# Kernel optimization log

Hardware: AMD Instinct MI355X
Metric: run time of the kernel (lower is better)

Reference implementation:

```python
import jax, jax.numpy as jnp
import numpy as np
import math

B, T, C, H = 4, 2048, 1024, 16
HS = C // H
EPS = 1e-5


def layernorm(x, g, b):
    mu = jnp.mean(x, axis=-1, keepdims=True)
    var = jnp.var(x, axis=-1, keepdims=True)
    return (x - mu) * jax.lax.rsqrt(var + EPS) * g + b


def setup_inputs() -> dict:
    key = jax.random.key(0)
    ks = jax.random.split(key, 7)
    rn = lambda k, s: jax.random.normal(k, s, dtype=jnp.float32) * 0.02
    return {
        "x": jax.random.normal(ks[0], (B, T, C), dtype=jnp.float32),
        "mask": jnp.tril(jnp.ones((T, T), dtype=jnp.int32)),  # causal tril buffer
        "wq": rn(ks[1], (H, HS, C)),  # stacked per-head Linear weights [out,in]
        "wk": rn(ks[2], (H, HS, C)),
        "wv": rn(ks[3], (H, HS, C)),
        "ln1_g": jnp.ones((C,), jnp.float32),
        "ln1_b": jnp.zeros((C,), jnp.float32),
        "ln2_g": jnp.ones((C,), jnp.float32),
        "ln2_b": jnp.zeros((C,), jnp.float32),
        "w1": rn(ks[4], (4 * C, C)),
        "b1": jnp.zeros((4 * C,), jnp.float32),
        "w2": rn(ks[5], (C, 4 * C)),
        "b2": jnp.zeros((C,), jnp.float32),
    }


def reference(x, mask, wq, wk, wv, ln1_g, ln1_b, ln2_g, ln2_b, w1, b1, w2, b2):
    Bx, Tx, Cx = x.shape
    h = layernorm(x, ln1_g, ln1_b)
    # per-head projections, batched over heads: [B,H,T,HS]
    q = jnp.einsum('btc,hdc->bhtd', h, wq)
    k = jnp.einsum('btc,hdc->bhtd', h, wk)
    v = jnp.einsum('btc,hdc->bhtd', h, wv)
    scores = jnp.einsum('bhtd,bhsd->bhts', q, k) * (1.0 / math.sqrt(HS))
    scores = jnp.where(mask[None, None, :Tx, :Tx] == 0, -jnp.inf, scores)
    w = jax.nn.softmax(scores, axis=-1)
    attn = jnp.einsum('bhts,bhsd->bhtd', w, v)  # [B,H,T,HS]
    attn = attn.transpose(0, 2, 1, 3).reshape(Bx, Tx, Cx)  # concat heads
    x = x + attn
    h2 = layernorm(x, ln2_g, ln2_b)
    ff = jax.nn.silu(h2 @ w1.T + b1) @ w2.T + b2  # dropout = identity (eval)
    return x + ff
```

## Files before the change

kernel.cpp:

```cpp
#include <hip/hip_runtime.h>
#include <stdint.h>

#define Bb 4
#define Tt 2048
#define Cc 1024
#define Hh 16
#define HSs 64

typedef __attribute__((ext_vector_type(8))) __bf16 bf16x8;
typedef __attribute__((ext_vector_type(4))) float f32x4;

__device__ __forceinline__ ushort f2bf(float f){
  union { float f; uint u; } c; c.f = f;
  uint r = c.u + 0x7fffu + ((c.u >> 16) & 1u);
  return (ushort)(r >> 16);
}
__device__ __forceinline__ float bf2f(ushort u){
  union { uint u; float f; } c; c.u = ((uint)u) << 16; return c.f;
}

__device__ __forceinline__ void gload16(const void* g, void* l){
  __builtin_amdgcn_global_load_lds(
      (__attribute__((address_space(1))) void*)(g),
      (__attribute__((address_space(3))) void*)(l), 16, 0, 0);
}

__global__ __launch_bounds__(256) void cast_bf16_kernel(const float* __restrict__ in,
                                                        ushort* __restrict__ out){
  int i = (blockIdx.x * 256 + threadIdx.x) * 4;
  float4 v = *(const float4*)(in + i);
  ushort4 o; o.x = f2bf(v.x); o.y = f2bf(v.y); o.z = f2bf(v.z); o.w = f2bf(v.w);
  *(ushort4*)(out + i) = o;
}

__global__ __launch_bounds__(256) void ln1_kernel(const float* __restrict__ x,
    const float* __restrict__ gw, const float* __restrict__ bw,
    ushort* __restrict__ hout){
  int row = blockIdx.x, tid = threadIdx.x;
  size_t base = (size_t)row * Cc + tid * 4;
  float4 xv = *(const float4*)(x + base);
  float s  = xv.x + xv.y + xv.z + xv.w;
  float ss = xv.x*xv.x + xv.y*xv.y + xv.z*xv.z + xv.w*xv.w;
  #pragma unroll
  for (int off = 1; off < 64; off <<= 1){ s += __shfl_xor(s, off); ss += __shfl_xor(ss, off); }
  __shared__ float red[8];
  int wid = tid >> 6, lane = tid & 63;
  if (lane == 0){ red[wid] = s; red[4 + wid] = ss; }
  __syncthreads();
  s  = red[0] + red[1] + red[2] + red[3];
  ss = red[4] + red[5] + red[6] + red[7];
  float mu = s * (1.0f / Cc);
  float rstd = rsqrtf(ss * (1.0f / Cc) - mu * mu + 1e-5f);
  float4 gv = *(const float4*)(gw + tid * 4);
  float4 bv = *(const float4*)(bw + tid * 4);
  ushort4 o;
  o.x = f2bf((xv.x - mu) * rstd * gv.x + bv.x);
  o.y = f2bf((xv.y - mu) * rstd * gv.y + bv.y);
  o.z = f2bf((xv.z - mu) * rstd * gv.z + bv.z);
  o.w = f2bf((xv.w - mu) * rstd * gv.w + bv.w);
  *(ushort4*)(hout + base) = o;
}

__global__ __launch_bounds__(256) void ln2_kernel(const float* __restrict__ x,
    const ushort* __restrict__ attnb,
    const float* __restrict__ gw, const float* __restrict__ bw,
    float* __restrict__ x2, ushort* __restrict__ hout){
  int row = blockIdx.x, tid = threadIdx.x;
  size_t base = (size_t)row * Cc + tid * 4;
  float4 xv = *(const float4*)(x + base);
  ushort4 av = *(const ushort4*)(attnb + base);
  xv.x += bf2f(av.x); xv.y += bf2f(av.y); xv.z += bf2f(av.z); xv.w += bf2f(av.w);
  *(float4*)(x2 + base) = xv;
  float s  = xv.x + xv.y + xv.z + xv.w;
  float ss = xv.x*xv.x + xv.y*xv.y + xv.z*xv.z + xv.w*xv.w;
  #pragma unroll
  for (int off = 1; off < 64; off <<= 1){ s += __shfl_xor(s, off); ss += __shfl_xor(ss, off); }
  __shared__ float red[8];
  int wid = tid >> 6, lane = tid & 63;
  if (lane == 0){ red[wid] = s; red[4 + wid] = ss; }
  __syncthreads();
  s  = red[0] + red[1] + red[2] + red[3];
  ss = red[4] + red[5] + red[6] + red[7];
  float mu = s * (1.0f / Cc);
  float rstd = rsqrtf(ss * (1.0f / Cc) - mu * mu + 1e-5f);
  float4 gv = *(const float4*)(gw + tid * 4);
  float4 bv = *(const float4*)(bw + tid * 4);
  ushort4 o;
  o.x = f2bf((xv.x - mu) * rstd * gv.x + bv.x);
  o.y = f2bf((xv.y - mu) * rstd * gv.y + bv.y);
  o.z = f2bf((xv.z - mu) * rstd * gv.z + bv.z);
  o.w = f2bf((xv.w - mu) * rstd * gv.w + bv.w);
  *(ushort4*)(hout + base) = o;
}

#define MFMA_QUAD(SI, QI, BQ) \
  { \
    _Pragma("unroll") \
    for (int mi = 0; mi < 4; ++mi){ \
      acc[(SI)*4+mi][(QI)*2+0] = __builtin_amdgcn_mfma_f32_16x16x32_bf16(af[mi][0], BQ[0][0], acc[(SI)*4+mi][(QI)*2+0], 0,0,0); \
      acc[(SI)*4+mi][(QI)*2+0] = __builtin_amdgcn_mfma_f32_16x16x32_bf16(af[mi][1], BQ[0][1], acc[(SI)*4+mi][(QI)*2+0], 0,0,0); \
      acc[(SI)*4+mi][(QI)*2+1] = __builtin_amdgcn_mfma_f32_16x16x32_bf16(af[mi][0], BQ[1][0], acc[(SI)*4+mi][(QI)*2+1], 0,0,0); \
      acc[(SI)*4+mi][(QI)*2+1] = __builtin_amdgcn_mfma_f32_16x16x32_bf16(af[mi][1], BQ[1][1], acc[(SI)*4+mi][(QI)*2+1], 0,0,0); \
    } \
  }

#define PH_SYNC_PRE()  { __builtin_amdgcn_sched_barrier(0); __builtin_amdgcn_s_barrier(); \
                         asm volatile("s_waitcnt lgkmcnt(0)" ::: "memory"); \
                         __builtin_amdgcn_sched_barrier(0); __builtin_amdgcn_s_setprio(1); }
#define PH_SYNC_POST() { __builtin_amdgcn_s_setprio(0); __builtin_amdgcn_sched_barrier(0); \
                         __builtin_amdgcn_s_barrier(); }

template<int MODE>
__global__ __launch_bounds__(512, 2) void gemm256_kernel(
    const ushort* __restrict__ A, const ushort* __restrict__ Bw,
    int N, int K,
    ushort* __restrict__ obf, float* __restrict__ of32,
    const float* __restrict__ bias)
{
  __shared__ __align__(16) ushort lds[2][2][2][128 * 64];
  int tid = threadIdx.x, lane = tid & 63, wid = tid >> 6;
  int wm = wid >> 2, wn = wid & 3;
  int c = lane & 15, g = lane >> 4;

  int nwg = gridDim.x, bid = blockIdx.x;
  int wgid = (bid & 7) * (nwg >> 3) + (bid >> 3);
  int m0, n0, koff = 0;
  if (MODE == 3){
    int split = wgid >> 7, rem = wgid & 127;
    m0 = (rem >> 2) << 8; n0 = (rem & 3) << 8; koff = split << 11;
  } else {
    int nTn = N >> 8;
    m0 = (wgid / nTn) << 8; n0 = (wgid % nTn) << 8;
  }

  const ushort* Ag = A  + (size_t)m0 * K + koff;
  const ushort* Bg = Bw + (size_t)n0 * K + koff;

  auto stage = [&](const ushort* gbase, int t, int ab, int h){
    #pragma unroll
    for (int j = 0; j < 2; ++j){
      int d = j * 8192 + wid * 1024 + lane * 16;
      int row = d >> 7;
      int colb = (d & 127) ^ ((row & 7) << 4);
      gload16((const char*)gbase + ((size_t)(h * 128 + row) * K + t * 64) * 2 + colb,
              (char*)&lds[t & 1][ab][h][0] + j * 8192 + wid * 1024);
    }
  };

  f32x4 acc[8][4] = {};
  bf16x8 af[4][2], bq0[2][2], bq1[2][2];
  int nt = (MODE == 3) ? (K >> 7) : (K >> 6);

  stage(Ag, 0, 0, 0); stage(Ag, 0, 0, 1);
  stage(Bg, 0, 1, 0); stage(Bg, 0, 1, 1);
  stage(Bg, 1, 1, 0); stage(Bg, 1, 1, 1);
  asm volatile("s_waitcnt vmcnt(4)" ::: "memory");
  __builtin_amdgcn_sched_barrier(0);
  __builtin_amdgcn_s_barrier();

  for (int t = 0; t < nt; ++t){
    const char* Abuf = (const char*)&lds[t & 1][0][wm][0];
    const char* Bbuf = (const char*)&lds[t & 1][1][wn >> 1][0];
    int brow0 = (wn & 1) * 64;

    #pragma unroll
    for (int mi = 0; mi < 4; ++mi){
      int row = mi * 16 + c, sw = (row & 7) << 4;
      af[mi][0] = *(const bf16x8*)(Abuf + row * 128 + ((g * 16) ^ sw));
      af[mi][1] = *(const bf16x8*)(Abuf + row * 128 + ((64 + g * 16) ^ sw));
    }
    #pragma unroll
    for (int nj = 0; nj < 2; ++nj){
      int row = brow0 + nj * 16 + c, sw = (row & 7) << 4;
      bq0[nj][0] = *(const bf16x8*)(Bbuf + row * 128 + ((g * 16) ^ sw));
      bq0[nj][1] = *(const bf16x8*)(Bbuf + row * 128 + ((64 + g * 16) ^ sw));
    }
    if (t + 1 < nt) stage(Ag, t + 1, 0, 0);
    PH_SYNC_PRE();
    MFMA_QUAD(0, 0, bq0);
    PH_SYNC_POST();

    #pragma unroll
    for (int nj = 0; nj < 2; ++nj){
      int row = brow0 + 32 + nj * 16 + c, sw = (row & 7) << 4;
      bq1[nj][0] = *(const bf16x8*)(Bbuf + row * 128 + ((g * 16) ^ sw));
      bq1[nj][1] = *(const bf16x8*)(Bbuf + row * 128 + ((64 + g * 16) ^ sw));
    }
    if (t + 1 < nt) stage(Ag, t + 1, 0, 1);
    PH_SYNC_PRE();
    MFMA_QUAD(0, 1, bq1);
    PH_SYNC_POST();

    #pragma unroll
    for (int mi = 0; mi < 4; ++mi){
      int row = 64 + mi * 16 + c, sw = (row & 7) << 4;
      af[mi][0] = *(const bf16x8*)(Abuf + row * 128 + ((g * 16) ^ sw));
      af[mi][1] = *(const bf16x8*)(Abuf + row * 128 + ((64 + g * 16) ^ sw));
    }
    if (t + 2 < nt) stage(Bg, t + 2, 1, 0);
    PH_SYNC_PRE();
    MFMA_QUAD(1, 0, bq0);
    PH_SYNC_POST();

    if (t + 2 < nt){
      stage(Bg, t + 2, 1, 1);
      asm volatile("s_waitcnt vmcnt(4)" ::: "memory");
    } else {
      asm volatile("s_waitcnt vmcnt(0)" ::: "memory");
    }
    __builtin_amdgcn_sched_barrier(0);
    __builtin_amdgcn_s_barrier();
    __builtin_amdgcn_s_setprio(1);
    MFMA_QUAD(1, 1, bq1);
    PH_SYNC_POST();
  }

  #pragma unroll
  for (int mi = 0; mi < 8; ++mi){
    #pragma unroll
    for (int ni = 0; ni < 4; ++ni){
      #pragma unroll
      for (int r = 0; r < 4; ++r){
        float v = acc[mi][ni][r];
        int m = m0 + wm * 128 + mi * 16 + g * 4 + r;
        int n = n0 + wn * 64 + ni * 16 + c;
        if (MODE == 0){
          int which = n >> 10;
          int nn = n & 1023;
          int b = m >> 11, t = m & (Tt - 1);
          int h = nn >> 6, d = nn & 63;
          float vv = (which == 0) ? v * 0.125f : v;
          size_t base = (size_t)which * (size_t)(Bb * Tt * Cc);
          size_t idx = (which == 2)
              ? ((((size_t)(b * Hh + h)) * HSs + d) * Tt + t)
              : ((((size_t)(b * Hh + h)) * Tt + t) * HSs + d);
          obf[base + idx] = f2bf(vv);
        } else if (MODE == 1){
          v += bias[n];
          float sv = v / (1.0f + __expf(-v));
          obf[(size_t)m * N + n] = f2bf(sv);
        } else {
          if (koff == 0) v += bias[n];
          atomicAdd(&of32[(size_t)m * N + n], v);
        }
      }
    }
  }
}

__global__ __launch_bounds__(256, 2) void attn_kernel(
    const ushort* __restrict__ q, const ushort* __restrict__ k,
    const ushort* __restrict__ vt, ushort* __restrict__ attnb)
{
  __shared__ __align__(16) ushort Ksm[3][64 * 64];
  __shared__ __align__(16) ushort Vsm[3][64 * 64];
  __shared__ __align__(16) ushort Pl[4][32 * 64];

  int bh  = blockIdx.y;
  int p   = blockIdx.x;
  int tid = threadIdx.x, wid = tid >> 6, lane = tid & 63;
  int g = lane >> 4, c = lane & 15;
  int qbA = 15 - p, qbB = p;
  int q0A = qbA * 128 + wid * 32;
  int q0B = qbB * 128 + wid * 32;
  const ushort* Qb = q  + (size_t)bh * Tt * HSs;
  const ushort* Kb = k  + (size_t)bh * Tt * HSs;
  const ushort* Vt = vt + (size_t)bh * HSs * Tt;
  char* Pw = (char*)&Pl[wid][0];

  auto stageKV = [&](int bsel, int s0){
    #pragma unroll
    for (int half = 0; half < 2; ++half){
      int i = wid + half * 4;
      int row = i * 8 + (lane >> 3);
      int col = ((lane & 7) ^ (row & 7)) * 8;
      gload16(Kb + (size_t)(s0 + row) * HSs + col, &Ksm[bsel][i * 512]);
      gload16(Vt + (size_t)row * Tt + s0 + col,    &Vsm[bsel][i * 512]);
    }
  };

  bf16x8 qfA[2][2], qfB[2][2];
  #pragma unroll
  for (int mi = 0; mi < 2; ++mi)
    #pragma unroll
    for (int ks = 0; ks < 2; ++ks){
      qfA[mi][ks] = *(const bf16x8*)(Qb + (size_t)(q0A + mi * 16 + c) * HSs + ks * 32 + g * 8);
      qfB[mi][ks] = *(const bf16x8*)(Qb + (size_t)(q0B + mi * 16 + c) * HSs + ks * 32 + g * 8);
    }

  f32x4 oA[2][4] = {}, oB[2][4] = {};
  float mA[2][4], lA[2][4], mB[2][4], lB[2][4];
  #pragma unroll
  for (int mi = 0; mi < 2; ++mi)
    #pragma unroll
    for (int r = 0; r < 4; ++r){
      mA[mi][r] = -1e30f; lA[mi][r] = 0.f;
      mB[mi][r] = -1e30f; lB[mi][r] = 0.f;
    }

  auto computeTile = [&](bf16x8 (&qf)[2][2], f32x4 (&o)[2][4],
                         float (&mrow)[2][4], float (&lpart)[2][4],
                         int q0w, int s0, const char* Kbuf, const char* Vbuf){
    f32x4 S[2][4] = {};
    bf16x8 kf[4][2];
    #pragma unroll
    for (int ni = 0; ni < 4; ++ni)
      #pragma unroll
      for (int ks = 0; ks < 2; ++ks)
        kf[ni][ks] = *(const bf16x8*)(Kbuf + (ni * 16 + c) * 128 + (((ks * 4 + g) ^ (c & 7)) << 4));
    #pragma unroll
    for (int mi = 0; mi < 2; ++mi)
      #pragma unroll
      for (int ni = 0; ni < 4; ++ni)
        #pragma unroll
        for (int ks = 0; ks < 2; ++ks)
          S[mi][ni] = __builtin_amdgcn_mfma_f32_16x16x32_bf16(qf[mi][ks], kf[ni][ks], S[mi][ni], 0, 0, 0);

    if (s0 + 63 > q0w){
      #pragma unroll
      for (int mi = 0; mi < 2; ++mi)
        #pragma unroll
        for (int ni = 0; ni < 4; ++ni)
          #pragma unroll
          for (int r = 0; r < 4; ++r){
            int tl = q0w + mi * 16 + g * 4 + r, sl = s0 + ni * 16 + c;
            if (sl > tl) S[mi][ni][r] = -1e30f;
          }
    }

    float lmax[2][4], worst = -1e30f;
    #pragma unroll
    for (int mi = 0; mi < 2; ++mi)
      #pragma unroll
      for (int r = 0; r < 4; ++r){
        float a0 = fmaxf(S[mi][0][r], S[mi][1][r]);
        float a1 = fmaxf(S[mi][2][r], S[mi][3][r]);
        lmax[mi][r] = fmaxf(a0, a1);
        worst = fmaxf(worst, lmax[mi][r] - mrow[mi][r]);
      }
    if (!__all(worst <= 8.0f)){
      #pragma unroll
      for (int mi = 0; mi < 2; ++mi)
        #pragma unroll
        for (int r = 0; r < 4; ++r){
          float mx = lmax[mi][r];
          mx = fmaxf(mx, __shfl_xor(mx, 1));
          mx = fmaxf(mx, __shfl_xor(mx, 2));
          mx = fmaxf(mx, __shfl_xor(mx, 4));
          mx = fmaxf(mx, __shfl_xor(mx, 8));
          float mnew  = fmaxf(mrow[mi][r], mx);
          float alpha = __expf(mrow[mi][r] - mnew);
          lpart[mi][r] *= alpha;
          #pragma unroll
          for (int dt = 0; dt < 4; ++dt) o[mi][dt][r] *= alpha;
          mrow[mi][r] = mnew;
        }
    }
    #pragma unroll
    for (int mi = 0; mi < 2; ++mi)
      #pragma unroll
      for (int r = 0; r < 4; ++r){
        int row = mi * 16 + g * 4 + r;
        float mb = mrow[mi][r] * 1.44269504f;
        float pp[4];
        #pragma unroll
        for (int ni = 0; ni < 4; ++ni){
          pp[ni] = exp2f(__builtin_fmaf(S[mi][ni][r], 1.44269504f, -mb));
          *(ushort*)(Pw + row * 128 + (((ni * 32 + 2 * c) ^ ((row & 7) << 4)))) = f2bf(pp[ni]);
        }
        lpart[mi][r] += (pp[0] + pp[1]) + (pp[2] + pp[3]);
      }
    __builtin_amdgcn_sched_barrier(0);

    bf16x8 vf[4][2];
    #pragma unroll
    for (int dt = 0; dt < 4; ++dt)
      #pragma unroll
      for (int ks = 0; ks < 2; ++ks)
        vf[dt][ks] = *(const bf16x8*)(Vbuf + (dt * 16 + c) * 128 + (((ks * 4 + g) ^ (c & 7)) << 4));
    #pragma unroll
    for (int mi = 0; mi < 2; ++mi){
      #pragma unroll
      for (int ks = 0; ks < 2; ++ks){
        bf16x8 pf = *(const bf16x8*)(Pw + (mi * 16 + c) * 128 + ((((ks * 4 + g) ^ (c & 7)) << 4)));
        #pragma unroll
        for (int dt = 0; dt < 4; ++dt)
          o[mi][dt] = __builtin_amdgcn_mfma_f32_16x16x32_bf16(pf, vf[dt][ks], o[mi][dt], 0, 0, 0);
      }
    }
    __builtin_amdgcn_sched_barrier(0);
  };

  int nchA = 2 * qbA + 2;

  stageKV(0, 0);
  stageKV(1, 64);
  asm volatile("s_waitcnt vmcnt(4)" ::: "memory");
  __builtin_amdgcn_sched_barrier(0);
  __builtin_amdgcn_s_barrier();

  int bufC = 0;
  for (int ch = 0; ch < nchA; ++ch){
    int s0 = ch * 64;
    bool staged = (ch + 2 < nchA);
    if (staged) stageKV((bufC == 0) ? 2 : bufC - 1, s0 + 128);

    const char* Kbuf = (const char*)&Ksm[bufC][0];
    const char* Vbuf = (const char*)&Vsm[bufC][0];
    if (s0 <= q0A + 31)
      computeTile(qfA, oA, mA, lA, q0A, s0, Kbuf, Vbuf);
    if (s0 <= q0B + 31)
      computeTile(qfB, oB, mB, lB, q0B, s0, Kbuf, Vbuf);

    if (staged) asm volatile("s_waitcnt vmcnt(4)" ::: "memory");
    else        asm volatile("s_waitcnt vmcnt(0)" ::: "memory");
    __builtin_amdgcn_sched_barrier(0);
    __builtin_amdgcn_s_barrier();
    bufC = (bufC == 2) ? 0 : bufC + 1;
  }

  int b = bh >> 4, h = bh & 15;
  #pragma unroll
  for (int mi = 0; mi < 2; ++mi)
    #pragma unroll
    for (int r = 0; r < 4; ++r){
      float la = lA[mi][r];
      la += __shfl_xor(la, 1); la += __shfl_xor(la, 2);
      la += __shfl_xor(la, 4); la += __shfl_xor(la, 8);
      float lia = 1.0f / la;
      float lb = lB[mi][r];
      lb += __shfl_xor(lb, 1); lb += __shfl_xor(lb, 2);
      lb += __shfl_xor(lb, 4); lb += __shfl_xor(lb, 8);
      float lib = 1.0f / lb;
      #pragma unroll
      for (int dt = 0; dt < 4; ++dt){
        int tA = q0A + mi * 16 + g * 4 + r;
        int tB = q0B + mi * 16 + g * 4 + r;
        attnb[((size_t)(b * Tt + tA)) * Cc + h * HSs + dt * 16 + c] = f2bf(oA[mi][dt][r] * lia);
        attnb[((size_t)(b * Tt + tB)) * Cc + h * HSs + dt * 16 + c] = f2bf(oB[mi][dt][r] * lib);
      }
    }
}

extern "C" void kernel_launch(void* const* d_in, const int* in_sizes, int n_in,
                              void* d_out, int out_size, void* d_ws, size_t ws_size,
                              hipStream_t stream) {
  (void)in_sizes; (void)n_in; (void)out_size; (void)ws_size;
  const float* x    = (const float*)d_in[0];
  const float* wq   = (const float*)d_in[2];
  const float* wk   = (const float*)d_in[3];
  const float* wv   = (const float*)d_in[4];
  const float* ln1g = (const float*)d_in[5];
  const float* ln1b = (const float*)d_in[6];
  const float* ln2g = (const float*)d_in[7];
  const float* ln2b = (const float*)d_in[8];
  const float* w1   = (const float*)d_in[9];
  const float* b1   = (const float*)d_in[10];
  const float* w2   = (const float*)d_in[11];
  const float* b2   = (const float*)d_in[12];
  float* out = (float*)d_out;

  char* ws = (char*)d_ws;
  const size_t SZ_ACT = (size_t)Bb * Tt * Cc * 2;
  ushort* h1    = (ushort*)(ws);
  ushort* qbuf  = (ushort*)(ws + SZ_ACT);
  ushort* kbuf  = (ushort*)(ws + 2 * SZ_ACT);
  ushort* vbuf  = (ushort*)(ws + 3 * SZ_ACT);
  ushort* attnb = (ushort*)(ws + 4 * SZ_ACT);
  ushort* h2    = (ushort*)(ws + 5 * SZ_ACT);
  ushort* h3    = (ushort*)(ws + 6 * SZ_ACT);
  char*   wsw   = ws + 6 * SZ_ACT + (size_t)Bb * Tt * 4 * Cc * 2;
  ushort* wqb = (ushort*)(wsw);
  ushort* wkb = (ushort*)(wsw + (size_t)Cc * Cc * 2);
  ushort* wvb = (ushort*)(wsw + 2 * (size_t)Cc * Cc * 2);
  ushort* w1b = (ushort*)(wsw + 3 * (size_t)Cc * Cc * 2);
  ushort* w2b = (ushort*)(wsw + 3 * (size_t)Cc * Cc * 2 + (size_t)4 * Cc * Cc * 2);

  cast_bf16_kernel<<<dim3(Cc * Cc / 1024), 256, 0, stream>>>(wq, wqb);
  cast_bf16_kernel<<<dim3(Cc * Cc / 1024), 256, 0, stream>>>(wk, wkb);
  cast_bf16_kernel<<<dim3(Cc * Cc / 1024), 256, 0, stream>>>(wv, wvb);
  cast_bf16_kernel<<<dim3(4 * Cc * Cc / 1024), 256, 0, stream>>>(w1, w1b);
  cast_bf16_kernel<<<dim3(4 * Cc * Cc / 1024), 256, 0, stream>>>(w2, w2b);

  ln1_kernel<<<dim3(Bb * Tt), 256, 0, stream>>>(x, ln1g, ln1b, h1);

  gemm256_kernel<0><<<dim3(32 * 12), 512, 0, stream>>>(h1, wqb, 3 * Cc, Cc, qbuf, nullptr, nullptr);

  attn_kernel<<<dim3(8, Bb * Hh), 256, 0, stream>>>(qbuf, kbuf, vbuf, attnb);

  ln2_kernel<<<dim3(Bb * Tt), 256, 0, stream>>>(x, attnb, ln2g, ln2b, out, h2);

  gemm256_kernel<1><<<dim3(32 * 16), 512, 0, stream>>>(h2, w1b, 4 * Cc, Cc, h3, nullptr, b1);
  gemm256_kernel<3><<<dim3(256), 512, 0, stream>>>(h3, w2b, Cc, 4 * Cc, nullptr, out, b2);
}
```

Baseline: 426.5 us.

## Merge weight casts into one kernel, split FFN1 GEMM, drop attention sched barriers

```diff
diff --git a/kernel.cpp b/kernel.cpp
--- a/kernel.cpp
+++ b/kernel.cpp
@@ -25,10 +25,18 @@
       (__attribute__((address_space(3))) void*)(l), 16, 0, 0);
 }
 
-__global__ __launch_bounds__(256) void cast_bf16_kernel(const float* __restrict__ in,
-                                                        ushort* __restrict__ out){
+__global__ __launch_bounds__(256) void cast_all_kernel(
+    const float* __restrict__ wq, const float* __restrict__ wk,
+    const float* __restrict__ wv, const float* __restrict__ w1,
+    const float* __restrict__ w2, ushort* __restrict__ out){
   int i = (blockIdx.x * 256 + threadIdx.x) * 4;
-  float4 v = *(const float4*)(in + i);
+  const float* src; int off;
+  if      (i <  1048576){ src = wq; off = i; }
+  else if (i <  2097152){ src = wk; off = i - 1048576; }
+  else if (i <  3145728){ src = wv; off = i - 2097152; }
+  else if (i <  7340032){ src = w1; off = i - 3145728; }
+  else                  { src = w2; off = i - 7340032; }
+  float4 v = *(const float4*)(src + off);
   ushort4 o; o.x = f2bf(v.x); o.y = f2bf(v.y); o.z = f2bf(v.z); o.w = f2bf(v.w);
   *(ushort4*)(out + i) = o;
 }
@@ -111,9 +119,9 @@
                          __builtin_amdgcn_s_barrier(); }
 
 template<int MODE>
-__global__ __launch_bounds__(512, 2) void gemm256_kernel(
+__device__ __forceinline__ void gemm256_body(
     const ushort* __restrict__ A, const ushort* __restrict__ Bw,
-    int N, int K,
+    int N, int K, int ldO,
     ushort* __restrict__ obf, float* __restrict__ of32,
     const float* __restrict__ bias)
 {
@@ -238,7 +246,7 @@
         } else if (MODE == 1){
           v += bias[n];
           float sv = v / (1.0f + __expf(-v));
-          obf[(size_t)m * N + n] = f2bf(sv);
+          obf[(size_t)m * ldO + n] = f2bf(sv);
         } else {
           if (koff == 0) v += bias[n];
           atomicAdd(&of32[(size_t)m * N + n], v);
@@ -246,6 +254,22 @@
       }
     }
   }
+}
+
+__global__ __launch_bounds__(512, 2) void gemm_qkv_kernel(
+    const ushort* __restrict__ A, const ushort* __restrict__ Bw, int N, int K,
+    ushort* __restrict__ obf){
+  gemm256_body<0>(A, Bw, N, K, 0, obf, nullptr, nullptr);
+}
+__global__ __launch_bounds__(512, 2) void gemm_ffn1_kernel(
+    const ushort* __restrict__ A, const ushort* __restrict__ Bw, int N, int K, int ldO,
+    ushort* __restrict__ obf, const float* __restrict__ bias){
+  gemm256_body<1>(A, Bw, N, K, ldO, obf, nullptr, bias);
+}
+__global__ __launch_bounds__(512, 2) void gemm_ffn2_kernel(
+    const ushort* __restrict__ A, const ushort* __restrict__ Bw, int N, int K,
+    float* __restrict__ of32, const float* __restrict__ bias){
+  gemm256_body<3>(A, Bw, N, K, N, nullptr, of32, bias);
 }
 
 __global__ __launch_bounds__(256, 2) void attn_kernel(
@@ -370,7 +394,6 @@
         }
         lpart[mi][r] += (pp[0] + pp[1]) + (pp[2] + pp[3]);
       }
-    __builtin_amdgcn_sched_barrier(0);
 
     bf16x8 vf[4][2];
     #pragma unroll
@@ -388,7 +411,6 @@
           o[mi][dt] = __builtin_amdgcn_mfma_f32_16x16x32_bf16(pf, vf[dt][ks], o[mi][dt], 0, 0, 0);
       }
     }
-    __builtin_amdgcn_sched_barrier(0);
   };
 
   int nchA = 2 * qbA + 2;
@@ -471,25 +493,20 @@
   ushort* h3    = (ushort*)(ws + 6 * SZ_ACT);
   char*   wsw   = ws + 6 * SZ_ACT + (size_t)Bb * Tt * 4 * Cc * 2;
   ushort* wqb = (ushort*)(wsw);
-  ushort* wkb = (ushort*)(wsw + (size_t)Cc * Cc * 2);
-  ushort* wvb = (ushort*)(wsw + 2 * (size_t)Cc * Cc * 2);
   ushort* w1b = (ushort*)(wsw + 3 * (size_t)Cc * Cc * 2);
   ushort* w2b = (ushort*)(wsw + 3 * (size_t)Cc * Cc * 2 + (size_t)4 * Cc * Cc * 2);
 
-  cast_bf16_kernel<<<dim3(Cc * Cc / 1024), 256, 0, stream>>>(wq, wqb);
-  cast_bf16_kernel<<<dim3(Cc * Cc / 1024), 256, 0, stream>>>(wk, wkb);
-  cast_bf16_kernel<<<dim3(Cc * Cc / 1024), 256, 0, stream>>>(wv, wvb);
-  cast_bf16_kernel<<<dim3(4 * Cc * Cc / 1024), 256, 0, stream>>>(w1, w1b);
-  cast_bf16_kernel<<<dim3(4 * Cc * Cc / 1024), 256, 0, stream>>>(w2, w2b);
+  cast_all_kernel<<<dim3(11264), 256, 0, stream>>>(wq, wk, wv, w1, w2, wqb);
 
   ln1_kernel<<<dim3(Bb * Tt), 256, 0, stream>>>(x, ln1g, ln1b, h1);
 
-  gemm256_kernel<0><<<dim3(32 * 12), 512, 0, stream>>>(h1, wqb, 3 * Cc, Cc, qbuf, nullptr, nullptr);
+  gemm_qkv_kernel<<<dim3(32 * 12), 512, 0, stream>>>(h1, wqb, 3 * Cc, Cc, qbuf);
 
   attn_kernel<<<dim3(8, Bb * Hh), 256, 0, stream>>>(qbuf, kbuf, vbuf, attnb);
 
   ln2_kernel<<<dim3(Bb * Tt), 256, 0, stream>>>(x, attnb, ln2g, ln2b, out, h2);
 
-  gemm256_kernel<1><<<dim3(32 * 16), 512, 0, stream>>>(h2, w1b, 4 * Cc, Cc, h3, nullptr, b1);
-  gemm256_kernel<3><<<dim3(256), 512, 0, stream>>>(h3, w2b, Cc, 4 * Cc, nullptr, out, b2);
-}
+  gemm_ffn1_kernel<<<dim3(32 * 8), 512, 0, stream>>>(h2, w1b,                      2048, Cc, 4 * Cc, h3,        b1);
+  gemm_ffn1_kernel<<<dim3(32 * 8), 512, 0, stream>>>(h2, w1b + (size_t)2048 * Cc,  2048, Cc, 4 * Cc, h3 + 2048, b1 + 2048);
+  gemm_ffn2_kernel<<<dim3(256), 512, 0, stream>>>(h3, w2b, Cc, 4 * Cc, out, b2);
+}
```

After: 421.7 us. Within noise of the previous version (-1.1%).
